# Optimization experiments

Hardware: AMD Instinct MI355X
Metric: run time of the kernel (lower is better)

The kernel has to match this reference:

```python
import jax, jax.numpy as jnp
import numpy as np

B, S, D, H = 2, 2048, 1024, 16
DK = D // H


def setup_inputs() -> dict:
    key = jax.random.key(0)
    ks = jax.random.split(key, 8)
    Q = jax.random.normal(ks[0], (B, S, D), dtype=jnp.float32)
    K = jax.random.normal(ks[1], (B, S, D), dtype=jnp.float32)
    V = jax.random.normal(ks[2], (B, S, D), dtype=jnp.float32)
    scale = 0.02
    W_q = jax.random.normal(ks[3], (D, D), dtype=jnp.float32) * scale
    W_k = jax.random.normal(ks[4], (D, D), dtype=jnp.float32) * scale
    W_v = jax.random.normal(ks[5], (D, D), dtype=jnp.float32) * scale
    W_o = jax.random.normal(ks[6], (D, D), dtype=jnp.float32) * scale
    b_q = jnp.zeros((D,), jnp.float32)
    b_k = jnp.zeros((D,), jnp.float32)
    b_v = jnp.zeros((D,), jnp.float32)
    b_o = jnp.zeros((D,), jnp.float32)
    # causal mask, broadcastable [1,1,S,S]; mask==0 positions are masked out
    mask = jnp.tril(jnp.ones((S, S), jnp.int32))[None, None, :, :]
    return dict(Q=Q, K=K, V=V, W_q=W_q, b_q=b_q, W_k=W_k, b_k=b_k,
                W_v=W_v, b_v=b_v, W_o=W_o, b_o=b_o, mask=mask)


def reference(Q, K, V, W_q, b_q, W_k, b_k, W_v, b_v, W_o, b_o, mask):
    # linear projections (torch Linear equivalent up to weight layout)
    q = Q @ W_q + b_q   # [B,S,D]
    k = K @ W_k + b_k
    v = V @ W_v + b_v
    # split heads -> [B,H,S,DK]
    q = q.reshape(B, S, H, DK).transpose(0, 2, 1, 3)
    k = k.reshape(B, S, H, DK).transpose(0, 2, 1, 3)
    v = v.reshape(B, S, H, DK).transpose(0, 2, 1, 3)
    # scaled dot-product attention with explicit [B,H,S,S] scores
    scores = jnp.einsum('bhqd,bhkd->bhqk', q, k) / jnp.sqrt(jnp.float32(DK))
    scores = jnp.where(mask == 0, jnp.float32(-1e9), scores)
    attn = jax.nn.softmax(scores, axis=-1)
    out = jnp.einsum('bhqk,bhkd->bhqd', attn, v)
    # merge heads and output projection
    out = out.transpose(0, 2, 1, 3).reshape(B, S, D)
    return out @ W_o + b_o
```

## Files before the change

kernel.cpp:

```cpp
#include <hip/hip_runtime.h>


typedef unsigned short u16;
typedef __attribute__((ext_vector_type(8))) short s8v;
typedef __attribute__((ext_vector_type(4))) float f4v;

#define S_ 2048
#define D_ 1024
#define H_ 16
#define DK_ 64

__device__ __forceinline__ u16 f2bf(float f) {
  unsigned u = __builtin_bit_cast(unsigned, f);
  u += 0x7fffu + ((u >> 16) & 1u);
  return (u16)(u >> 16);
}
__device__ __forceinline__ u16 f2bf_t(float f) {
  return (u16)(__builtin_bit_cast(unsigned, f) >> 16);
}

__device__ __forceinline__ void gld_lds16(const u16* g, u16* l) {
  __builtin_amdgcn_global_load_lds(
      (const __attribute__((address_space(1))) unsigned int*)g,
      (__attribute__((address_space(3))) unsigned int*)l, 16, 0, 0);
}

__global__ __launch_bounds__(256) void cast3_bf16(
    const float* __restrict__ s0, const float* __restrict__ s1, const float* __restrict__ s2,
    u16* __restrict__ d0, u16* __restrict__ d1, u16* __restrict__ d2, int n4) {
  const float* s = blockIdx.y == 0 ? s0 : blockIdx.y == 1 ? s1 : s2;
  u16*         d = blockIdx.y == 0 ? d0 : blockIdx.y == 1 ? d1 : d2;
  int i = blockIdx.x * 256 + threadIdx.x;
  int stride = gridDim.x * 256;
  for (int idx = i; idx < n4; idx += stride) {
    float4 f = ((const float4*)s)[idx];
    unsigned lo = (unsigned)f2bf(f.x) | ((unsigned)f2bf(f.y) << 16);
    unsigned hi = (unsigned)f2bf(f.z) | ((unsigned)f2bf(f.w) << 16);
    ((uint2*)d)[idx] = make_uint2(lo, hi);
  }
}

__global__ __launch_bounds__(256) void wtrans(
    const float* __restrict__ W0, const float* __restrict__ W1,
    const float* __restrict__ W2, const float* __restrict__ W3,
    u16* __restrict__ T0, u16* __restrict__ T1, u16* __restrict__ T2, u16* __restrict__ T3) {
  int z = blockIdx.z;
  const float* W = z == 0 ? W0 : z == 1 ? W1 : z == 2 ? W2 : W3;
  u16*         T = z == 0 ? T0 : z == 1 ? T1 : z == 2 ? T2 : T3;
  __shared__ float tile[32][33];
  int tx = threadIdx.x & 31, ty = threadIdx.x >> 5;
  int c0 = blockIdx.x * 32, r0 = blockIdx.y * 32;
#pragma unroll
  for (int i = 0; i < 32; i += 8)
    tile[ty + i][tx] = W[(size_t)(r0 + ty + i) * D_ + c0 + tx];
  __syncthreads();
#pragma unroll
  for (int i = 0; i < 32; i += 8)
    T[(size_t)(c0 + ty + i) * D_ + r0 + tx] = f2bf(tile[tx][ty + i]);
}

#define BM_ 128
#define BN_ 64
#define BK_ 64

__device__ __forceinline__ void gemm_core(const u16* __restrict__ A, const u16* __restrict__ Bt,
                                          const float* __restrict__ bias, void* __restrict__ out,
                                          int mode) {
  __shared__ __attribute__((aligned(16))) u16 lds[BM_ * BK_ + BN_ * BK_];
  u16* Al = lds;
  u16* Bl = lds + BM_ * BK_;
  int tid = threadIdx.x;
  int w = tid >> 6, lane = tid & 63, quad = lane >> 4, col = lane & 15;
  int wm = (w >> 1) * 64, wn = (w & 1) * 32;
  int m0 = blockIdx.y * BM_, n0 = blockIdx.x * BN_;
  f4v acc[4][2] = {};
  const u16* Ag = A + (size_t)m0 * 1024;
  const u16* Bg = Bt + (size_t)n0 * 1024;
  int sr = tid >> 3, ss = tid & 7;

  for (int k0 = 0; k0 < 1024; k0 += BK_) {
    __syncthreads();
#pragma unroll
    for (int c = 0; c < 4; ++c) {
      int r = c * 32 + sr;
      int gs = ss ^ (r & 7);
      gld_lds16(Ag + (size_t)r * 1024 + k0 + gs * 8, &Al[r * BK_ + ss * 8]);
    }
#pragma unroll
    for (int c = 0; c < 2; ++c) {
      int r = c * 32 + sr;
      int gs = ss ^ (r & 7);
      gld_lds16(Bg + (size_t)r * 1024 + k0 + gs * 8, &Bl[r * BK_ + ss * 8]);
    }
    __syncthreads();
#pragma unroll
    for (int hf = 0; hf < 2; ++hf) {
      s8v af[4], bfr[2];
#pragma unroll
      for (int i = 0; i < 4; ++i) {
        int row = wm + i * 16 + col;
        int sl = (hf * 4 + quad) ^ (row & 7);
        af[i] = *(const s8v*)&Al[row * BK_ + sl * 8];
      }
#pragma unroll
      for (int j = 0; j < 2; ++j) {
        int row = wn + j * 16 + col;
        int sl = (hf * 4 + quad) ^ (row & 7);
        bfr[j] = *(const s8v*)&Bl[row * BK_ + sl * 8];
      }
#pragma unroll
      for (int i = 0; i < 4; ++i)
#pragma unroll
        for (int j = 0; j < 2; ++j)
          acc[i][j] = __builtin_amdgcn_mfma_f32_16x16x32_bf16(af[i], bfr[j], acc[i][j], 0, 0, 0);
    }
  }

  if (mode == 1) {
    __syncthreads();
    u16* sc = lds + w * (32 * 72);
#pragma unroll
    for (int j = 0; j < 2; ++j) {
      int n = n0 + wn + j * 16 + col;
      float bb = bias[n];
#pragma unroll
      for (int i = 0; i < 4; ++i)
#pragma unroll
        for (int r = 0; r < 4; ++r)
          sc[(j * 16 + col) * 72 + i * 16 + quad * 4 + r] = f2bf(acc[i][j][r] + bb);
    }
    __builtin_amdgcn_wave_barrier();
    int dkl = lane & 31, sh = (lane >> 5) * 32;
    int h = n0 >> 6;
    int dkg = wn + dkl;
    int mg0 = m0 + wm + sh;
    int b = mg0 >> 11, s0g = mg0 & 2047;
    u16* op = (u16*)out + ((size_t)(b * H_ + h) * DK_ + dkg) * S_ + s0g;
#pragma unroll
    for (int c = 0; c < 4; ++c)
      *(uint4*)&op[c * 8] = *(const uint4*)&sc[dkl * 72 + sh + c * 8];
    return;
  }

#pragma unroll
  for (int i = 0; i < 4; ++i) {
#pragma unroll
    for (int j = 0; j < 2; ++j) {
      int n = n0 + wn + j * 16 + col;
      float bb = bias[n];
#pragma unroll
      for (int r = 0; r < 4; ++r) {
        int m = m0 + wm + i * 16 + quad * 4 + r;
        float v = acc[i][j][r] + bb;
        if (mode == 2) {
          ((float*)out)[(size_t)m * 1024 + n] = v;
        } else {
          int b = m >> 11, s = m & 2047, h = n >> 6, dk = n & 63;
          ((u16*)out)[((size_t)(b * H_ + h) * S_ + s) * DK_ + dk] = f2bf(v);
        }
      }
    }
  }
}

__global__ __launch_bounds__(256, 5) void gemm_qkv(
    const u16* __restrict__ A0, const u16* __restrict__ A1, const u16* __restrict__ A2,
    const u16* __restrict__ B0, const u16* __restrict__ B1, const u16* __restrict__ B2,
    const float* __restrict__ bi0, const float* __restrict__ bi1, const float* __restrict__ bi2,
    u16* __restrict__ o0, u16* __restrict__ o1, u16* __restrict__ o2) {
  int z = blockIdx.z;
  const u16* A = z == 0 ? A0 : z == 1 ? A1 : A2;
  const u16* Bt = z == 0 ? B0 : z == 1 ? B1 : B2;
  const float* bias = z == 0 ? bi0 : z == 1 ? bi1 : bi2;
  u16* o = z == 0 ? o0 : z == 1 ? o1 : o2;
  gemm_core(A, Bt, bias, o, z == 2 ? 1 : 0);
}

__global__ __launch_bounds__(256, 5) void gemm_out(const u16* __restrict__ A, const u16* __restrict__ Bt,
                                                   const float* __restrict__ bias, float* __restrict__ out) {
  gemm_core(A, Bt, bias, out, 2);
}

#define QB_ 64
#define KT_ 64
#define PSTR 72

__global__ __launch_bounds__(256) void attn_fused(const u16* __restrict__ qb, const u16* __restrict__ kb,
                                                  const u16* __restrict__ vtb, u16* __restrict__ ao) {
  __shared__ __attribute__((aligned(16))) u16 Kt[KT_ * PSTR];
  __shared__ __attribute__((aligned(16))) u16 Vts[DK_ * PSTR];
  __shared__ __attribute__((aligned(16))) u16 Pl[4][16 * PSTR];
  int bh = blockIdx.y, b = bh >> 4, h = bh & 15;
  int tid = threadIdx.x, w = tid >> 6, lane = tid & 63, quad = lane >> 4, col = lane & 15;
  const u16* Qh = qb + (size_t)bh * S_ * DK_;
  const u16* Kh = kb + (size_t)bh * S_ * DK_;
  const u16* Vh = vtb + (size_t)bh * DK_ * S_;
  int krow = tid >> 3, kcol = (tid & 7) * 8;
  const float CEXP = 0.18033688f;

  for (int ph = 0; ph < 2; ++ph) {
    int qi = ph ? (int)blockIdx.x : 31 - (int)blockIdx.x;
    int qbase = qi * QB_;
    int wave_qmin = qbase + w * 16;
    int wave_qmax = wave_qmin + 15;
    int nk = qbase + QB_;

    s8v qf0 = *(const s8v*)(Qh + (size_t)(wave_qmin + col) * DK_ + quad * 8);
    s8v qf1 = *(const s8v*)(Qh + (size_t)(wave_qmin + col) * DK_ + 32 + quad * 8);

    f4v O[4] = {};
    float lsum[4] = {};

    uint4 k0r = *(const uint4*)(Kh + (size_t)krow * DK_ + kcol);
    uint4 k1r = *(const uint4*)(Kh + (size_t)(32 + krow) * DK_ + kcol);
    uint4 v0r = *(const uint4*)(Vh + (size_t)krow * S_ + kcol);
    uint4 v1r = *(const uint4*)(Vh + (size_t)(32 + krow) * S_ + kcol);

    for (int kt = 0; kt < nk; kt += KT_) {
      __syncthreads();
      *(uint4*)&Kt[krow * PSTR + kcol] = k0r;
      *(uint4*)&Kt[(32 + krow) * PSTR + kcol] = k1r;
      *(uint4*)&Vts[krow * PSTR + kcol] = v0r;
      *(uint4*)&Vts[(32 + krow) * PSTR + kcol] = v1r;
      __syncthreads();
      int kn = kt + KT_;
      if (kn < nk) {
        k0r = *(const uint4*)(Kh + (size_t)(kn + krow) * DK_ + kcol);
        k1r = *(const uint4*)(Kh + (size_t)(kn + 32 + krow) * DK_ + kcol);
        v0r = *(const uint4*)(Vh + (size_t)krow * S_ + kn + kcol);
        v1r = *(const uint4*)(Vh + (size_t)(32 + krow) * S_ + kn + kcol);
      }
      if (kt > wave_qmax) continue;

      f4v sc[4];
#pragma unroll
      for (int ks = 0; ks < 4; ++ks) {
        s8v kf0 = *(const s8v*)&Kt[(ks * 16 + col) * PSTR + quad * 8];
        s8v kf1 = *(const s8v*)&Kt[(ks * 16 + col) * PSTR + 32 + quad * 8];
        f4v t = {0.f, 0.f, 0.f, 0.f};
        t = __builtin_amdgcn_mfma_f32_16x16x32_bf16(qf0, kf0, t, 0, 0, 0);
        t = __builtin_amdgcn_mfma_f32_16x16x32_bf16(qf1, kf1, t, 0, 0, 0);
        sc[ks] = t;
      }

      bool full = (kt + KT_ - 1 <= wave_qmin);
#pragma unroll
      for (int r = 0; r < 4; ++r) {
        float p0, p1, p2, p3;
        if (full) {
          p0 = exp2f(sc[0][r] * CEXP);
          p1 = exp2f(sc[1][r] * CEXP);
          p2 = exp2f(sc[2][r] * CEXP);
          p3 = exp2f(sc[3][r] * CEXP);
        } else {
          int qr = wave_qmin + quad * 4 + r;
          p0 = (kt + col)      <= qr ? exp2f(sc[0][r] * CEXP) : 0.f;
          p1 = (kt + 16 + col) <= qr ? exp2f(sc[1][r] * CEXP) : 0.f;
          p2 = (kt + 32 + col) <= qr ? exp2f(sc[2][r] * CEXP) : 0.f;
          p3 = (kt + 48 + col) <= qr ? exp2f(sc[3][r] * CEXP) : 0.f;
        }
        lsum[r] += (p0 + p1) + (p2 + p3);
        int row = quad * 4 + r;
        Pl[w][row * PSTR + col]      = f2bf_t(p0);
        Pl[w][row * PSTR + 16 + col] = f2bf_t(p1);
        Pl[w][row * PSTR + 32 + col] = f2bf_t(p2);
        Pl[w][row * PSTR + 48 + col] = f2bf_t(p3);
      }
      __builtin_amdgcn_wave_barrier();

      s8v pa0 = *(const s8v*)&Pl[w][col * PSTR + quad * 8];
      s8v pa1 = *(const s8v*)&Pl[w][col * PSTR + 32 + quad * 8];
#pragma unroll
      for (int d = 0; d < 4; ++d) {
        s8v vf0 = *(const s8v*)&Vts[(d * 16 + col) * PSTR + quad * 8];
        s8v vf1 = *(const s8v*)&Vts[(d * 16 + col) * PSTR + 32 + quad * 8];
        O[d] = __builtin_amdgcn_mfma_f32_16x16x32_bf16(pa0, vf0, O[d], 0, 0, 0);
        O[d] = __builtin_amdgcn_mfma_f32_16x16x32_bf16(pa1, vf1, O[d], 0, 0, 0);
      }
    }

#pragma unroll
    for (int r = 0; r < 4; ++r) {
      float l = lsum[r];
      l += __shfl_xor(l, 1);
      l += __shfl_xor(l, 2);
      l += __shfl_xor(l, 4);
      l += __shfl_xor(l, 8);
      float inv = 1.0f / l;
      size_t row = (size_t)(b * S_ + wave_qmin + quad * 4 + r);
#pragma unroll
      for (int d = 0; d < 4; ++d)
        ao[row * D_ + h * DK_ + d * 16 + col] = f2bf(O[d][r] * inv);
    }
  }
}

extern "C" void kernel_launch(void* const* d_in, const int* in_sizes, int n_in,
                              void* d_out, int out_size, void* d_ws, size_t ws_size,
                              hipStream_t stream) {
  const float* Q  = (const float*)d_in[0];
  const float* K  = (const float*)d_in[1];
  const float* V  = (const float*)d_in[2];
  const float* Wq = (const float*)d_in[3];
  const float* bq = (const float*)d_in[4];
  const float* Wk = (const float*)d_in[5];
  const float* bk = (const float*)d_in[6];
  const float* Wv = (const float*)d_in[7];
  const float* bv = (const float*)d_in[8];
  const float* Wo = (const float*)d_in[9];
  const float* bo = (const float*)d_in[10];

  char* p = (char*)d_ws;
  const size_t TEN = (size_t)2 * S_ * D_ * 2;
  const size_t WT  = (size_t)D_ * D_ * 2;
  u16* Qc  = (u16*)p; p += TEN;
  u16* Kc  = (u16*)p; p += TEN;
  u16* Vc  = (u16*)p; p += TEN;
  u16* Wqt = (u16*)p; p += WT;
  u16* Wkt = (u16*)p; p += WT;
  u16* Wvt = (u16*)p; p += WT;
  u16* Wot = (u16*)p; p += WT;
  u16* qb  = (u16*)p; p += TEN;
  u16* kbf = (u16*)p; p += TEN;
  u16* vtb = (u16*)p; p += TEN;
  u16* ao  = (u16*)p; p += TEN;

  cast3_bf16<<<dim3(1024, 3), 256, 0, stream>>>(Q, K, V, Qc, Kc, Vc, (2 * S_ * D_) / 4);
  wtrans<<<dim3(32, 32, 4), 256, 0, stream>>>(Wq, Wk, Wv, Wo, Wqt, Wkt, Wvt, Wot);
  gemm_qkv<<<dim3(D_ / BN_, 32, 3), 256, 0, stream>>>(Qc, Kc, Vc, Wqt, Wkt, Wvt, bq, bk, bv, qb, kbf, vtb);
  attn_fused<<<dim3(16, 2 * H_), 256, 0, stream>>>(qb, kbf, vtb, ao);
  gemm_out<<<dim3(D_ / BN_, 32), 256, 0, stream>>>(ao, Wot, bo, (float*)d_out);
}
```

Before: 243.0 us.

## Merge prep kernels, fold softmax scale into Q projection, share K/V tiles across query blocks

After: 251.4 us. 1.03x slower.

```diff
diff --git a/kernel.cpp b/kernel.cpp
--- a/kernel.cpp
+++ b/kernel.cpp
@@ -25,38 +25,40 @@
       (__attribute__((address_space(3))) unsigned int*)l, 16, 0, 0);
 }
 
-__global__ __launch_bounds__(256) void cast3_bf16(
-    const float* __restrict__ s0, const float* __restrict__ s1, const float* __restrict__ s2,
-    u16* __restrict__ d0, u16* __restrict__ d1, u16* __restrict__ d2, int n4) {
-  const float* s = blockIdx.y == 0 ? s0 : blockIdx.y == 1 ? s1 : s2;
-  u16*         d = blockIdx.y == 0 ? d0 : blockIdx.y == 1 ? d1 : d2;
-  int i = blockIdx.x * 256 + threadIdx.x;
-  int stride = gridDim.x * 256;
-  for (int idx = i; idx < n4; idx += stride) {
-    float4 f = ((const float4*)s)[idx];
-    unsigned lo = (unsigned)f2bf(f.x) | ((unsigned)f2bf(f.y) << 16);
-    unsigned hi = (unsigned)f2bf(f.z) | ((unsigned)f2bf(f.w) << 16);
-    ((uint2*)d)[idx] = make_uint2(lo, hi);
-  }
-}
-
-__global__ __launch_bounds__(256) void wtrans(
+__global__ __launch_bounds__(256) void prep(
+    const float* __restrict__ Q, const float* __restrict__ K, const float* __restrict__ V,
+    u16* __restrict__ Qc, u16* __restrict__ Kc, u16* __restrict__ Vc,
     const float* __restrict__ W0, const float* __restrict__ W1,
     const float* __restrict__ W2, const float* __restrict__ W3,
     u16* __restrict__ T0, u16* __restrict__ T1, u16* __restrict__ T2, u16* __restrict__ T3) {
-  int z = blockIdx.z;
-  const float* W = z == 0 ? W0 : z == 1 ? W1 : z == 2 ? W2 : W3;
-  u16*         T = z == 0 ? T0 : z == 1 ? T1 : z == 2 ? T2 : T3;
-  __shared__ float tile[32][33];
-  int tx = threadIdx.x & 31, ty = threadIdx.x >> 5;
-  int c0 = blockIdx.x * 32, r0 = blockIdx.y * 32;
-#pragma unroll
-  for (int i = 0; i < 32; i += 8)
-    tile[ty + i][tx] = W[(size_t)(r0 + ty + i) * D_ + c0 + tx];
-  __syncthreads();
-#pragma unroll
-  for (int i = 0; i < 32; i += 8)
-    T[(size_t)(c0 + ty + i) * D_ + r0 + tx] = f2bf(tile[tx][ty + i]);
+  int bid = blockIdx.x, tid = threadIdx.x;
+  if (bid < 3072) {
+    int z = bid >> 10, t = bid & 1023;
+    const float* s = z == 0 ? Q : z == 1 ? K : V;
+    u16*         d = z == 0 ? Qc : z == 1 ? Kc : Vc;
+    const int n4 = (2 * S_ * D_) / 4;
+    for (int idx = t * 256 + tid; idx < n4; idx += 1024 * 256) {
+      float4 f = ((const float4*)s)[idx];
+      unsigned lo = (unsigned)f2bf(f.x) | ((unsigned)f2bf(f.y) << 16);
+      unsigned hi = (unsigned)f2bf(f.z) | ((unsigned)f2bf(f.w) << 16);
+      ((uint2*)d)[idx] = make_uint2(lo, hi);
+    }
+  } else {
+    int wb = bid - 3072;
+    int z = wb >> 10, t = wb & 1023;
+    const float* W = z == 0 ? W0 : z == 1 ? W1 : z == 2 ? W2 : W3;
+    u16*         T = z == 0 ? T0 : z == 1 ? T1 : z == 2 ? T2 : T3;
+    __shared__ float tile[32][33];
+    int tx = tid & 31, ty = tid >> 5;
+    int c0 = (t & 31) * 32, r0 = (t >> 5) * 32;
+#pragma unroll
+    for (int i = 0; i < 32; i += 8)
+      tile[ty + i][tx] = W[(size_t)(r0 + ty + i) * D_ + c0 + tx];
+    __syncthreads();
+#pragma unroll
+    for (int i = 0; i < 32; i += 8)
+      T[(size_t)(c0 + ty + i) * D_ + r0 + tx] = f2bf(tile[tx][ty + i]);
+  }
 }
 
 #define BM_ 128
@@ -65,7 +67,7 @@
 
 __device__ __forceinline__ void gemm_core(const u16* __restrict__ A, const u16* __restrict__ Bt,
                                           const float* __restrict__ bias, void* __restrict__ out,
-                                          int mode) {
+                                          int mode, float oscale) {
   __shared__ __attribute__((aligned(16))) u16 lds[BM_ * BK_ + BN_ * BK_];
   u16* Al = lds;
   u16* Bl = lds + BM_ * BK_;
@@ -151,7 +153,7 @@
 #pragma unroll
       for (int r = 0; r < 4; ++r) {
         int m = m0 + wm + i * 16 + quad * 4 + r;
-        float v = acc[i][j][r] + bb;
+        float v = (acc[i][j][r] + bb) * oscale;
         if (mode == 2) {
           ((float*)out)[(size_t)m * 1024 + n] = v;
         } else {
@@ -163,7 +165,9 @@
   }
 }
 
-__global__ __launch_bounds__(256, 5) void gemm_qkv(
+#define CEXPQ 0.18033688f
+
+__global__ __launch_bounds__(256, 4) void gemm_qkv(
     const u16* __restrict__ A0, const u16* __restrict__ A1, const u16* __restrict__ A2,
     const u16* __restrict__ B0, const u16* __restrict__ B1, const u16* __restrict__ B2,
     const float* __restrict__ bi0, const float* __restrict__ bi1, const float* __restrict__ bi2,
@@ -173,15 +177,14 @@
   const u16* Bt = z == 0 ? B0 : z == 1 ? B1 : B2;
   const float* bias = z == 0 ? bi0 : z == 1 ? bi1 : bi2;
   u16* o = z == 0 ? o0 : z == 1 ? o1 : o2;
-  gemm_core(A, Bt, bias, o, z == 2 ? 1 : 0);
-}
-
-__global__ __launch_bounds__(256, 5) void gemm_out(const u16* __restrict__ A, const u16* __restrict__ Bt,
+  gemm_core(A, Bt, bias, o, z == 2 ? 1 : 0, z == 0 ? CEXPQ : 1.0f);
+}
+
+__global__ __launch_bounds__(256, 4) void gemm_out(const u16* __restrict__ A, const u16* __restrict__ Bt,
                                                    const float* __restrict__ bias, float* __restrict__ out) {
-  gemm_core(A, Bt, bias, out, 2);
-}
-
-#define QB_ 64
+  gemm_core(A, Bt, bias, out, 2, 1.0f);
+}
+
 #define KT_ 64
 #define PSTR 72
 
@@ -191,75 +194,82 @@
   __shared__ __attribute__((aligned(16))) u16 Vts[DK_ * PSTR];
   __shared__ __attribute__((aligned(16))) u16 Pl[4][16 * PSTR];
   int bh = blockIdx.y, b = bh >> 4, h = bh & 15;
+  int j = blockIdx.x;
+  int lo_base = j * 64, hi_base = (31 - j) * 64;
   int tid = threadIdx.x, w = tid >> 6, lane = tid & 63, quad = lane >> 4, col = lane & 15;
   const u16* Qh = qb + (size_t)bh * S_ * DK_;
   const u16* Kh = kb + (size_t)bh * S_ * DK_;
   const u16* Vh = vtb + (size_t)bh * DK_ * S_;
   int krow = tid >> 3, kcol = (tid & 7) * 8;
-  const float CEXP = 0.18033688f;
-
-  for (int ph = 0; ph < 2; ++ph) {
-    int qi = ph ? (int)blockIdx.x : 31 - (int)blockIdx.x;
-    int qbase = qi * QB_;
-    int wave_qmin = qbase + w * 16;
-    int wave_qmax = wave_qmin + 15;
-    int nk = qbase + QB_;
-
-    s8v qf0 = *(const s8v*)(Qh + (size_t)(wave_qmin + col) * DK_ + quad * 8);
-    s8v qf1 = *(const s8v*)(Qh + (size_t)(wave_qmin + col) * DK_ + 32 + quad * 8);
-
-    f4v O[4] = {};
-    float lsum[4] = {};
-
-    uint4 k0r = *(const uint4*)(Kh + (size_t)krow * DK_ + kcol);
-    uint4 k1r = *(const uint4*)(Kh + (size_t)(32 + krow) * DK_ + kcol);
-    uint4 v0r = *(const uint4*)(Vh + (size_t)krow * S_ + kcol);
-    uint4 v1r = *(const uint4*)(Vh + (size_t)(32 + krow) * S_ + kcol);
-
-    for (int kt = 0; kt < nk; kt += KT_) {
-      __syncthreads();
-      *(uint4*)&Kt[krow * PSTR + kcol] = k0r;
-      *(uint4*)&Kt[(32 + krow) * PSTR + kcol] = k1r;
-      *(uint4*)&Vts[krow * PSTR + kcol] = v0r;
-      *(uint4*)&Vts[(32 + krow) * PSTR + kcol] = v1r;
-      __syncthreads();
-      int kn = kt + KT_;
-      if (kn < nk) {
-        k0r = *(const uint4*)(Kh + (size_t)(kn + krow) * DK_ + kcol);
-        k1r = *(const uint4*)(Kh + (size_t)(kn + 32 + krow) * DK_ + kcol);
-        v0r = *(const uint4*)(Vh + (size_t)krow * S_ + kn + kcol);
-        v1r = *(const uint4*)(Vh + (size_t)(32 + krow) * S_ + kn + kcol);
-      }
-      if (kt > wave_qmax) continue;
-
+
+  int lo_qmin = lo_base + w * 16, hi_qmin = hi_base + w * 16;
+  s8v qlo0 = *(const s8v*)(Qh + (size_t)(lo_qmin + col) * DK_ + quad * 8);
+  s8v qlo1 = *(const s8v*)(Qh + (size_t)(lo_qmin + col) * DK_ + 32 + quad * 8);
+  s8v qhi0 = *(const s8v*)(Qh + (size_t)(hi_qmin + col) * DK_ + quad * 8);
+  s8v qhi1 = *(const s8v*)(Qh + (size_t)(hi_qmin + col) * DK_ + 32 + quad * 8);
+
+  f4v Olo[4] = {}, Ohi[4] = {};
+  float lslo[4] = {}, lshi[4] = {};
+
+  int nk = hi_base + 64;
+  uint4 k0r = *(const uint4*)(Kh + (size_t)krow * DK_ + kcol);
+  uint4 k1r = *(const uint4*)(Kh + (size_t)(32 + krow) * DK_ + kcol);
+  uint4 v0r = *(const uint4*)(Vh + (size_t)krow * S_ + kcol);
+  uint4 v1r = *(const uint4*)(Vh + (size_t)(32 + krow) * S_ + kcol);
+
+  for (int kt = 0; kt < nk; kt += KT_) {
+    __syncthreads();
+    *(uint4*)&Kt[krow * PSTR + kcol] = k0r;
+    *(uint4*)&Kt[(32 + krow) * PSTR + kcol] = k1r;
+    *(uint4*)&Vts[krow * PSTR + kcol] = v0r;
+    *(uint4*)&Vts[(32 + krow) * PSTR + kcol] = v1r;
+    __syncthreads();
+    int kn = kt + KT_;
+    if (kn < nk) {
+      k0r = *(const uint4*)(Kh + (size_t)(kn + krow) * DK_ + kcol);
+      k1r = *(const uint4*)(Kh + (size_t)(kn + 32 + krow) * DK_ + kcol);
+      v0r = *(const uint4*)(Vh + (size_t)krow * S_ + kn + kcol);
+      v1r = *(const uint4*)(Vh + (size_t)(32 + krow) * S_ + kn + kcol);
+    }
+
+    s8v kf[4][2], vf[4][2];
+#pragma unroll
+    for (int ks = 0; ks < 4; ++ks) {
+      kf[ks][0] = *(const s8v*)&Kt[(ks * 16 + col) * PSTR + quad * 8];
+      kf[ks][1] = *(const s8v*)&Kt[(ks * 16 + col) * PSTR + 32 + quad * 8];
+    }
+#pragma unroll
+    for (int d = 0; d < 4; ++d) {
+      vf[d][0] = *(const s8v*)&Vts[(d * 16 + col) * PSTR + quad * 8];
+      vf[d][1] = *(const s8v*)&Vts[(d * 16 + col) * PSTR + 32 + quad * 8];
+    }
+
+    auto process = [&](const s8v& q0, const s8v& q1, int qmin, f4v* O, float* ls) {
       f4v sc[4];
 #pragma unroll
       for (int ks = 0; ks < 4; ++ks) {
-        s8v kf0 = *(const s8v*)&Kt[(ks * 16 + col) * PSTR + quad * 8];
-        s8v kf1 = *(const s8v*)&Kt[(ks * 16 + col) * PSTR + 32 + quad * 8];
         f4v t = {0.f, 0.f, 0.f, 0.f};
-        t = __builtin_amdgcn_mfma_f32_16x16x32_bf16(qf0, kf0, t, 0, 0, 0);
-        t = __builtin_amdgcn_mfma_f32_16x16x32_bf16(qf1, kf1, t, 0, 0, 0);
+        t = __builtin_amdgcn_mfma_f32_16x16x32_bf16(q0, kf[ks][0], t, 0, 0, 0);
+        t = __builtin_amdgcn_mfma_f32_16x16x32_bf16(q1, kf[ks][1], t, 0, 0, 0);
         sc[ks] = t;
       }
-
-      bool full = (kt + KT_ - 1 <= wave_qmin);
+      bool full = (kt + KT_ - 1 <= qmin);
 #pragma unroll
       for (int r = 0; r < 4; ++r) {
         float p0, p1, p2, p3;
         if (full) {
-          p0 = exp2f(sc[0][r] * CEXP);
-          p1 = exp2f(sc[1][r] * CEXP);
-          p2 = exp2f(sc[2][r] * CEXP);
-          p3 = exp2f(sc[3][r] * CEXP);
+          p0 = exp2f(sc[0][r]);
+          p1 = exp2f(sc[1][r]);
+          p2 = exp2f(sc[2][r]);
+          p3 = exp2f(sc[3][r]);
         } else {
-          int qr = wave_qmin + quad * 4 + r;
-          p0 = (kt + col)      <= qr ? exp2f(sc[0][r] * CEXP) : 0.f;
-          p1 = (kt + 16 + col) <= qr ? exp2f(sc[1][r] * CEXP) : 0.f;
-          p2 = (kt + 32 + col) <= qr ? exp2f(sc[2][r] * CEXP) : 0.f;
-          p3 = (kt + 48 + col) <= qr ? exp2f(sc[3][r] * CEXP) : 0.f;
+          int qr = qmin + quad * 4 + r;
+          p0 = (kt + col)      <= qr ? exp2f(sc[0][r]) : 0.f;
+          p1 = (kt + 16 + col) <= qr ? exp2f(sc[1][r]) : 0.f;
+          p2 = (kt + 32 + col) <= qr ? exp2f(sc[2][r]) : 0.f;
+          p3 = (kt + 48 + col) <= qr ? exp2f(sc[3][r]) : 0.f;
         }
-        lsum[r] += (p0 + p1) + (p2 + p3);
+        ls[r] += (p0 + p1) + (p2 + p3);
         int row = quad * 4 + r;
         Pl[w][row * PSTR + col]      = f2bf_t(p0);
         Pl[w][row * PSTR + 16 + col] = f2bf_t(p1);
@@ -267,27 +277,35 @@
         Pl[w][row * PSTR + 48 + col] = f2bf_t(p3);
       }
       __builtin_amdgcn_wave_barrier();
-
       s8v pa0 = *(const s8v*)&Pl[w][col * PSTR + quad * 8];
       s8v pa1 = *(const s8v*)&Pl[w][col * PSTR + 32 + quad * 8];
 #pragma unroll
       for (int d = 0; d < 4; ++d) {
-        s8v vf0 = *(const s8v*)&Vts[(d * 16 + col) * PSTR + quad * 8];
-        s8v vf1 = *(const s8v*)&Vts[(d * 16 + col) * PSTR + 32 + quad * 8];
-        O[d] = __builtin_amdgcn_mfma_f32_16x16x32_bf16(pa0, vf0, O[d], 0, 0, 0);
-        O[d] = __builtin_amdgcn_mfma_f32_16x16x32_bf16(pa1, vf1, O[d], 0, 0, 0);
-      }
-    }
-
+        O[d] = __builtin_amdgcn_mfma_f32_16x16x32_bf16(pa0, vf[d][0], O[d], 0, 0, 0);
+        O[d] = __builtin_amdgcn_mfma_f32_16x16x32_bf16(pa1, vf[d][1], O[d], 0, 0, 0);
+      }
+      __builtin_amdgcn_wave_barrier();
+    };
+
+    process(qhi0, qhi1, hi_qmin, Ohi, lshi);
+    if (kt <= lo_qmin + 15)
+      process(qlo0, qlo1, lo_qmin, Olo, lslo);
+  }
+
+#pragma unroll
+  for (int g = 0; g < 2; ++g) {
+    f4v* O = g ? Olo : Ohi;
+    float* ls = g ? lslo : lshi;
+    int qmin = g ? lo_qmin : hi_qmin;
 #pragma unroll
     for (int r = 0; r < 4; ++r) {
-      float l = lsum[r];
+      float l = ls[r];
       l += __shfl_xor(l, 1);
       l += __shfl_xor(l, 2);
       l += __shfl_xor(l, 4);
       l += __shfl_xor(l, 8);
       float inv = 1.0f / l;
-      size_t row = (size_t)(b * S_ + wave_qmin + quad * 4 + r);
+      size_t row = (size_t)(b * S_ + qmin + quad * 4 + r);
 #pragma unroll
       for (int d = 0; d < 4; ++d)
         ao[row * D_ + h * DK_ + d * 16 + col] = f2bf(O[d][r] * inv);
@@ -325,8 +343,7 @@
   u16* vtb = (u16*)p; p += TEN;
   u16* ao  = (u16*)p; p += TEN;
 
-  cast3_bf16<<<dim3(1024, 3), 256, 0, stream>>>(Q, K, V, Qc, Kc, Vc, (2 * S_ * D_) / 4);
-  wtrans<<<dim3(32, 32, 4), 256, 0, stream>>>(Wq, Wk, Wv, Wo, Wqt, Wkt, Wvt, Wot);
+  prep<<<7168, 256, 0, stream>>>(Q, K, V, Qc, Kc, Vc, Wq, Wk, Wv, Wo, Wqt, Wkt, Wvt, Wot);
   gemm_qkv<<<dim3(D_ / BN_, 32, 3), 256, 0, stream>>>(Qc, Kc, Vc, Wqt, Wkt, Wvt, bq, bk, bv, qb, kbf, vtb);
   attn_fused<<<dim3(16, 2 * H_), 256, 0, stream>>>(qb, kbf, vtb, ao);
   gemm_out<<<dim3(D_ / BN_, 32), 256, 0, stream>>>(ao, Wot, bo, (float*)d_out);
```
